# Optimization experiments

Measured on AMD Instinct MI355X. Metric: run time of the kernel, lower is better.

The kernel has to match this reference:

```python
import jax, jax.numpy as jnp
import numpy as np

C = 64
D = C // 8  # query/key channels
B, H, W = 4, 64, 64


def setup_inputs() -> dict:
    key = jax.random.key(0)
    ks = jax.random.split(key, 8)
    x = jax.random.normal(ks[0], (B, C, H, W), dtype=jnp.float32)
    # 1x1 conv params (kernel squeezed to [out_ch, in_ch])
    sq = 1.0 / np.sqrt(C)
    Wq = jax.random.uniform(ks[1], (D, C), jnp.float32, -sq, sq)
    bq = jax.random.uniform(ks[2], (D,), jnp.float32, -sq, sq)
    Wk = jax.random.uniform(ks[3], (D, C), jnp.float32, -sq, sq)
    bk = jax.random.uniform(ks[4], (D,), jnp.float32, -sq, sq)
    Wv = jax.random.uniform(ks[5], (C, C), jnp.float32, -sq, sq)
    bv = jax.random.uniform(ks[6], (C,), jnp.float32, -sq, sq)
    # gamma is zero-initialized in the module; use a nonzero value so the
    # attention path actually contributes to the output.
    gamma = jax.random.normal(ks[7], (1,), dtype=jnp.float32)
    return {"x": x, "Wq": Wq, "bq": bq, "Wk": Wk, "bk": bk, "Wv": Wv, "bv": bv, "gamma": gamma}


def reference(x, Wq, bq, Wk, bk, Wv, bv, gamma):
    b, c, h, w = x.shape
    n = h * w
    xf = x.reshape(b, c, n)                                   # [B,C,N]
    q = jnp.einsum('dc,bcn->bdn', Wq, xf) + bq[None, :, None]  # [B,D,N]
    k = jnp.einsum('dc,bcn->bdn', Wk, xf) + bk[None, :, None]  # [B,D,N]
    v = jnp.einsum('ec,bcn->ben', Wv, xf) + bv[None, :, None]  # [B,C,N]
    energy = jnp.einsum('bdn,bdm->bnm', q, k)                  # [B,N,N] = Q^T K
    attn = jax.nn.softmax(energy, axis=-1)                     # softmax over keys m
    # out[b,c,n] = sum_m v[b,c,m] * attn[b,n,m]  (V @ attention^T in torch)
    out = jnp.einsum('bcm,bnm->bcn', v, attn).reshape(b, c, h, w)
    return gamma[0] * out + x
```

## Files before the change

### kernel.cpp

```cpp
#include <hip/hip_runtime.h>
#include <hip/hip_bf16.h>
#include <math.h>

#define BB 4
#define CC 64
#define DD 8
#define NN 4096
#define KS 8
#define KPS (NN / KS)
#define VSTR 516
#define KSTR 12
#define LOG2E 1.44269504088896340736f

typedef __attribute__((ext_vector_type(4))) short short4v;
typedef __attribute__((ext_vector_type(8))) short short8s;
typedef __attribute__((ext_vector_type(4))) unsigned short ushort4v;
typedef __attribute__((ext_vector_type(8))) unsigned short ushort8;
typedef __attribute__((ext_vector_type(16))) float f32x16;

#if defined(__HIP_DEVICE_COMPILE__)
  #if __has_builtin(__builtin_amdgcn_mfma_f32_32x32x8bf16_1k)
    #define MFMA32x8(A, B, C) __builtin_amdgcn_mfma_f32_32x32x8bf16_1k(A, B, C, 0, 0, 0)
  #elif __has_builtin(__builtin_amdgcn_mfma_f32_32x32x8_bf16)
    #define MFMA32x8(A, B, C) __builtin_amdgcn_mfma_f32_32x32x8_bf16(A, B, C, 0, 0, 0)
  #else
    #error "no 32x32x8 bf16 MFMA builtin in device pass"
  #endif
  #if __has_builtin(__builtin_amdgcn_exp2f)
    #define EXP2(x) __builtin_amdgcn_exp2f(x)
  #else
    #define EXP2(x) exp2f(x)
  #endif
#else
  static __device__ __host__ inline f32x16 MFMA32x8(short4v, short4v, f32x16 c) { return c; }
  #define EXP2(x) exp2f(x)
#endif

static __device__ inline f32x16 PVMFMA(short8s A, short8s B, f32x16 c) {
#if defined(__HIP_DEVICE_COMPILE__) && __has_builtin(__builtin_amdgcn_mfma_f32_32x32x16_bf16)
    typedef __attribute__((ext_vector_type(8))) __bf16 bf16x8;
    return __builtin_amdgcn_mfma_f32_32x32x16_bf16(
        __builtin_bit_cast(bf16x8, A), __builtin_bit_cast(bf16x8, B), c, 0, 0, 0);
#else
    union { short8s v; short4v h[2]; } a, b;
    a.v = A; b.v = B;
    return MFMA32x8(a.h[1], b.h[1], MFMA32x8(a.h[0], b.h[0], c));
#endif
}

static __device__ inline short4v pack4(float a, float b, float c, float d) {
    union { short4v s; __hip_bfloat162 h[2]; } u;
    u.h[0] = __float22bfloat162_rn(make_float2(a, b));
    u.h[1] = __float22bfloat162_rn(make_float2(c, d));
    return u.s;
}
static __device__ inline unsigned packu(float lo, float hi) {
    union { __hip_bfloat162 h; unsigned u; } t;
    t.h = __float22bfloat162_rn(make_float2(lo, hi));
    return t.u;
}

__global__ __launch_bounds__(64) void qkv_kernel(
    const float* __restrict__ x,  const float* __restrict__ Wq, const float* __restrict__ bq,
    const float* __restrict__ Wk, const float* __restrict__ bk,
    const float* __restrict__ Wv, const float* __restrict__ bv,
    unsigned short* __restrict__ qb, unsigned short* __restrict__ kb,
    unsigned short* __restrict__ vT)
{
    __shared__ unsigned short LQ[32 * 8];
    __shared__ unsigned short LK[32 * 8];

    int lane = threadIdx.x & 63;
    int l32 = lane & 31, h2 = lane >> 5;

    int blk = blockIdx.x;
    int b = blk & (BB - 1);
    int ng = blk >> 2;
    int n0 = ng * 32;

    const float* xb = x + (size_t)b * CC * NN + n0 + l32;
    short4v bf[8];
    #pragma unroll
    for (int s = 0; s < 8; ++s) {
        int c0 = s * 8 + 4 * h2;
        float x0 = xb[(size_t)(c0 + 0) * NN];
        float x1 = xb[(size_t)(c0 + 1) * NN];
        float x2 = xb[(size_t)(c0 + 2) * NN];
        float x3 = xb[(size_t)(c0 + 3) * NN];
        bf[s] = pack4(x0, x1, x2, x3);
    }

    #pragma unroll
    for (int rt = 0; rt < 2; ++rt) {
        short4v af[8];
        #pragma unroll
        for (int s = 0; s < 8; ++s) {
            float4 w4 = *(const float4*)(Wv + (size_t)(rt * 32 + l32) * CC + s * 8 + 4 * h2);
            af[s] = pack4(w4.x, w4.y, w4.z, w4.w);
        }
        f32x16 acc;
        #pragma unroll
        for (int r = 0; r < 16; ++r) acc[r] = 0.f;
        #pragma unroll
        for (int s = 0; s < 8; ++s)
            acc = MFMA32x8(af[s], bf[s], acc);
        #pragma unroll
        for (int r = 0; r < 16; ++r) {
            int row = rt * 32 + (r & 3) + 8 * (r >> 2) + 4 * h2;
            float val = acc[r] + bv[row];
            __hip_bfloat16 hv = __float2bfloat16(val);
            vT[((size_t)b * CC + row) * NN + n0 + l32] = *(unsigned short*)&hv;
        }
    }

    {
        short4v af[8];
        #pragma unroll
        for (int s = 0; s < 8; ++s) {
            float4 w4;
            if (l32 < 8) {
                w4 = *(const float4*)(Wq + (size_t)l32 * CC + s * 8 + 4 * h2);
            } else if (l32 < 16) {
                w4 = *(const float4*)(Wk + (size_t)(l32 - 8) * CC + s * 8 + 4 * h2);
            } else {
                w4 = make_float4(0.f, 0.f, 0.f, 0.f);
            }
            af[s] = pack4(w4.x, w4.y, w4.z, w4.w);
        }
        f32x16 acc;
        #pragma unroll
        for (int r = 0; r < 16; ++r) acc[r] = 0.f;
        #pragma unroll
        for (int s = 0; s < 8; ++s)
            acc = MFMA32x8(af[s], bf[s], acc);

        short4v qp = pack4((acc[0] + bq[0 + 4 * h2]) * LOG2E,
                           (acc[1] + bq[1 + 4 * h2]) * LOG2E,
                           (acc[2] + bq[2 + 4 * h2]) * LOG2E,
                           (acc[3] + bq[3 + 4 * h2]) * LOG2E);
        short4v kp = pack4(acc[4] + bk[0 + 4 * h2],
                           acc[5] + bk[1 + 4 * h2],
                           acc[6] + bk[2 + 4 * h2],
                           acc[7] + bk[3 + 4 * h2]);
        *(short4v*)(LQ + (size_t)l32 * 8 + 4 * h2) = qp;
        *(short4v*)(LK + (size_t)l32 * 8 + 4 * h2) = kp;
        __syncthreads();
        int rw = lane & 31;
        if (lane < 32) {
            ushort8 row = *(const ushort8*)(LQ + (size_t)rw * 8);
            *(ushort8*)(qb + ((size_t)b * NN + n0 + rw) * 8) = row;
        } else {
            ushort8 row = *(const ushort8*)(LK + (size_t)rw * 8);
            *(ushort8*)(kb + ((size_t)b * NN + n0 + rw) * 8) = row;
        }
    }
}

__global__ __launch_bounds__(512, 4) void flash_kernel(
    const unsigned short* __restrict__ qb, const unsigned short* __restrict__ kb,
    const unsigned short* __restrict__ vT, unsigned* __restrict__ accb,
    float* __restrict__ sbuf)
{
    __shared__ unsigned short VS[64 * VSTR];
    __shared__ unsigned short KL[512 * KSTR];
    int tid = threadIdx.x;
    int wave = tid >> 6, lane = tid & 63;
    int l32 = lane & 31, h2 = lane >> 5;

    int blk = blockIdx.x;
    int b = blk & (BB - 1);
    int qchunk = (blk >> 2) & 15;
    int split = blk >> 6;
    int n0 = qchunk * 256 + wave * 32;

    short4v qf = *(const short4v*)(qb + ((size_t)b * NN + n0 + l32) * DD + h2 * 4);

    const unsigned short* kbb = kb + (size_t)b * NN * DD;
    const unsigned short* vbb = vT + (size_t)b * CC * NN;
    int m0 = split * KPS;

    {
        int ch = tid >> 3, s8 = (tid & 7) * 8;
        const unsigned short* vg = vbb + (size_t)ch * NN + m0 + s8;
        ushort8 v[8];
        #pragma unroll
        for (int k = 0; k < 8; ++k) v[k] = *(const ushort8*)(vg + 64 * k);
        ushort8 kA = *(const ushort8*)(kbb + (size_t)(m0 + tid) * DD);

        unsigned short* vp = VS + (size_t)ch * VSTR + s8;
        #pragma unroll
        for (int k = 0; k < 8; ++k) {
            *(ushort4v*)(vp + 64 * k)     = *(ushort4v*)&v[k];
            *(ushort4v*)(vp + 64 * k + 4) = *((ushort4v*)&v[k] + 1);
        }
        unsigned short* p = KL + (size_t)tid * KSTR;
        *(ushort4v*)(p)     = *(ushort4v*)&kA;
        *(ushort4v*)(p + 4) = *((ushort4v*)&kA + 1);
    }
    __syncthreads();

    f32x16 o0, o1, zz;
    #pragma unroll
    for (int r = 0; r < 16; ++r) { o0[r] = 0.f; o1[r] = 0.f; zz[r] = 0.f; }
    float s0 = 0.f, s1 = 0.f, s2 = 0.f, s3 = 0.f;

    #pragma unroll
    for (int s = 0; s < 16; ++s) {
        short4v kf = *(const short4v*)(KL + (size_t)(s * 32 + l32) * KSTR + h2 * 4);
        f32x16 st = MFMA32x8(kf, qf, zz);
        float w[16];
        #pragma unroll
        for (int r = 0; r < 16; ++r) w[r] = EXP2(st[r]);
        s0 += (w[0] + w[1]) + (w[2] + w[3]);
        s1 += (w[4] + w[5]) + (w[6] + w[7]);
        s2 += (w[8] + w[9]) + (w[10] + w[11]);
        s3 += (w[12] + w[13]) + (w[14] + w[15]);

        union { short4v s; __hip_bfloat162 h[2]; } u[4];
        #pragma unroll
        for (int g = 0; g < 4; ++g) {
            u[g].h[0] = __float22bfloat162_rn(make_float2(w[4 * g],     w[4 * g + 1]));
            u[g].h[1] = __float22bfloat162_rn(make_float2(w[4 * g + 2], w[4 * g + 3]));
        }
        #pragma unroll
        for (int j = 0; j < 2; ++j) {
            int kb0 = s * 32 + j * 16 + h2 * 4;
            union { short8s v; short4v h[2]; } A, B0, B1;
            A.h[0] = u[2 * j].s;
            A.h[1] = u[2 * j + 1].s;
            B0.h[0] = *(const short4v*)(VS + (size_t)(l32)      * VSTR + kb0);
            B0.h[1] = *(const short4v*)(VS + (size_t)(l32)      * VSTR + kb0 + 8);
            B1.h[0] = *(const short4v*)(VS + (size_t)(32 + l32) * VSTR + kb0);
            B1.h[1] = *(const short4v*)(VS + (size_t)(32 + l32) * VSTR + kb0 + 8);
            o0 = PVMFMA(A.v, B0.v, o0);
            o1 = PVMFMA(A.v, B1.v, o1);
        }
    }

    unsigned* au = accb + (((size_t)((b * KS + split) * 128 + qchunk * 8 + wave)) << 10);
    #pragma unroll
    for (int r = 0; r < 16; ++r)
        au[r * 64 + lane] = packu(o0[r], o1[r]);

    float ssum = (s0 + s1) + (s2 + s3);
    ssum += __shfl_xor(ssum, 32);
    if (lane < 32)
        sbuf[(size_t)(b * KS + split) * NN + n0 + l32] = ssum;
}

__global__ __launch_bounds__(256) void norm_kernel(
    const unsigned* __restrict__ accb, const float* __restrict__ sbuf,
    const float* __restrict__ x, const float* __restrict__ gamma,
    float* __restrict__ out)
{
    __shared__ float tile[16 * 65];
    __shared__ float stl[16];
    int blk = blockIdx.x;
    int t = blk & 7;
    int uu = blk >> 3;
    int b = t & 3;
    int qpar = t >> 2;
    int qhalf = uu & 1;
    int sub = (uu >> 1) & 7;
    int qhi = uu >> 4;
    int qchunk = qhi * 2 + qpar;
    int g32 = qchunk * 8 + sub;
    int n0 = g32 * 32 + qhalf * 16;
    int tid = threadIdx.x;

    if (tid < 16) {
        float st = 0.f;
        #pragma unroll
        for (int sp = 0; sp < KS; ++sp)
            st += sbuf[(size_t)(b * KS + sp) * NN + n0 + tid];
        stl[tid] = 1.0f / st;
    }

    int spoff = tid >> 7;
    int u = tid & 127;
    int rl = u >> 4;
    int lane0 = (u & 15) * 4;

    float alo[4], ahi[4];
    #pragma unroll
    for (int e = 0; e < 4; ++e) { alo[e] = 0.f; ahi[e] = 0.f; }
    #pragma unroll
    for (int p = 0; p < 4; ++p) {
        int sp = p * 2 + spoff;
        const unsigned* base = accb + (((size_t)((b * KS + sp) * 128 + g32)) << 10)
                             + qhalf * 512;
        uint4 v = *(const uint4*)(base + u * 4);
        unsigned wv[4] = {v.x, v.y, v.z, v.w};
        #pragma unroll
        for (int e = 0; e < 4; ++e) {
            alo[e] += __uint_as_float(wv[e] << 16);
            ahi[e] += __uint_as_float(wv[e] & 0xFFFF0000u);
        }
    }

    #pragma unroll
    for (int e = 0; e < 4; ++e) {
        int lane = lane0 + e;
        int h2 = lane >> 5, l32 = lane & 31;
        int ql = (rl & 3) + 8 * ((rl >> 2) & 1) + 4 * h2;
        if (tid < 128) {
            tile[ql * 65 + l32]      = alo[e];
            tile[ql * 65 + 32 + l32] = ahi[e];
        }
    }
    __syncthreads();
    #pragma unroll
    for (int e = 0; e < 4; ++e) {
        int lane = lane0 + e;
        int h2 = lane >> 5, l32 = lane & 31;
        int ql = (rl & 3) + 8 * ((rl >> 2) & 1) + 4 * h2;
        if (tid >= 128) {
            tile[ql * 65 + l32]      += alo[e];
            tile[ql * 65 + 32 + l32] += ahi[e];
        }
    }
    __syncthreads();

    float gm = gamma[0];
    #pragma unroll
    for (int p2 = 0; p2 < 4; ++p2) {
        int idx = p2 * 256 + tid;
        int c = idx >> 4, ql = idx & 15;
        size_t xi = ((size_t)b * CC + c) * NN + n0 + ql;
        out[xi] = gm * tile[ql * 65 + c] * stl[ql] + x[xi];
    }
}

extern "C" void kernel_launch(void* const* d_in, const int* in_sizes, int n_in,
                              void* d_out, int out_size, void* d_ws, size_t ws_size,
                              hipStream_t stream)
{
    const float* x     = (const float*)d_in[0];
    const float* Wq    = (const float*)d_in[1];
    const float* bq    = (const float*)d_in[2];
    const float* Wk    = (const float*)d_in[3];
    const float* bk    = (const float*)d_in[4];
    const float* Wv    = (const float*)d_in[5];
    const float* bv    = (const float*)d_in[6];
    const float* gamma = (const float*)d_in[7];
    float* out = (float*)d_out;

    float* ws = (float*)d_ws;
    size_t off = 0;
    unsigned short* qb = (unsigned short*)(ws + off); off += (size_t)BB * NN * DD / 2 + 64;
    unsigned short* kb = (unsigned short*)(ws + off); off += (size_t)BB * NN * DD / 2 + 64;
    unsigned short* vT = (unsigned short*)(ws + off); off += (size_t)BB * CC * NN / 2 + 64;
    unsigned* accb = (unsigned*)(ws + off); off += (size_t)BB * KS * NN * CC / 2;
    float* sbuf = ws + off; off += (size_t)BB * KS * NN;

    qkv_kernel<<<BB * 128, 64, 0, stream>>>(x, Wq, bq, Wk, bk, Wv, bv, qb, kb, vT);
    flash_kernel<<<KS * 16 * BB, 512, 0, stream>>>(qb, kb, vT, accb, sbuf);
    norm_kernel<<<BB * 256, 256, 0, stream>>>(accb, sbuf, x, gamma, out);
}
```

Baseline: 96.09 us.

## Halve key splits, double-buffer K/V tiles, compute row sums via MFMA

Cuts the number of key splits from 8 to 4, so each flash block now handles two 512-key tiles. The second tile's global loads are issued before computing the first, and it goes into a second shared-memory buffer. Softmax row sums are now produced by an extra MFMA against a ones vector instead of scalar adds. This aims to reduce partial-accumulator traffic in the norm kernel and to hide load latency. In exchange it launches half as many blocks, uses twice the LDS per block (occupancy hint lowered to 2), and adds one MFMA per PV step.

```diff
diff --git a/kernel.cpp b/kernel.cpp
--- a/kernel.cpp
+++ b/kernel.cpp
@@ -6,7 +6,7 @@
 #define CC 64
 #define DD 8
 #define NN 4096
-#define KS 8
+#define KS 4
 #define KPS (NN / KS)
 #define VSTR 516
 #define KSTR 12
@@ -156,13 +156,13 @@
     }
 }
 
-__global__ __launch_bounds__(512, 4) void flash_kernel(
+__global__ __launch_bounds__(512, 2) void flash_kernel(
     const unsigned short* __restrict__ qb, const unsigned short* __restrict__ kb,
     const unsigned short* __restrict__ vT, unsigned* __restrict__ accb,
     float* __restrict__ sbuf)
 {
-    __shared__ unsigned short VS[64 * VSTR];
-    __shared__ unsigned short KL[512 * KSTR];
+    __shared__ unsigned short VS[2][64 * VSTR];
+    __shared__ unsigned short KL[2][512 * KSTR];
     int tid = threadIdx.x;
     int wave = tid >> 6, lane = tid & 63;
     int l32 = lane & 31, h2 = lane >> 5;
@@ -179,73 +179,101 @@
     const unsigned short* vbb = vT + (size_t)b * CC * NN;
     int m0 = split * KPS;
 
+    int ch = tid >> 3, s8 = (tid & 7) * 8;
+    const unsigned short* vg = vbb + (size_t)ch * NN + m0 + s8;
+
     {
-        int ch = tid >> 3, s8 = (tid & 7) * 8;
-        const unsigned short* vg = vbb + (size_t)ch * NN + m0 + s8;
         ushort8 v[8];
         #pragma unroll
         for (int k = 0; k < 8; ++k) v[k] = *(const ushort8*)(vg + 64 * k);
         ushort8 kA = *(const ushort8*)(kbb + (size_t)(m0 + tid) * DD);
 
-        unsigned short* vp = VS + (size_t)ch * VSTR + s8;
+        unsigned short* vp = VS[0] + (size_t)ch * VSTR + s8;
         #pragma unroll
         for (int k = 0; k < 8; ++k) {
             *(ushort4v*)(vp + 64 * k)     = *(ushort4v*)&v[k];
             *(ushort4v*)(vp + 64 * k + 4) = *((ushort4v*)&v[k] + 1);
         }
-        unsigned short* p = KL + (size_t)tid * KSTR;
+        unsigned short* p = KL[0] + (size_t)tid * KSTR;
         *(ushort4v*)(p)     = *(ushort4v*)&kA;
         *(ushort4v*)(p + 4) = *((ushort4v*)&kA + 1);
     }
     __syncthreads();
 
-    f32x16 o0, o1, zz;
-    #pragma unroll
-    for (int r = 0; r < 16; ++r) { o0[r] = 0.f; o1[r] = 0.f; zz[r] = 0.f; }
-    float s0 = 0.f, s1 = 0.f, s2 = 0.f, s3 = 0.f;
-
-    #pragma unroll
-    for (int s = 0; s < 16; ++s) {
-        short4v kf = *(const short4v*)(KL + (size_t)(s * 32 + l32) * KSTR + h2 * 4);
-        f32x16 st = MFMA32x8(kf, qf, zz);
-        float w[16];
-        #pragma unroll
-        for (int r = 0; r < 16; ++r) w[r] = EXP2(st[r]);
-        s0 += (w[0] + w[1]) + (w[2] + w[3]);
-        s1 += (w[4] + w[5]) + (w[6] + w[7]);
-        s2 += (w[8] + w[9]) + (w[10] + w[11]);
-        s3 += (w[12] + w[13]) + (w[14] + w[15]);
-
-        union { short4v s; __hip_bfloat162 h[2]; } u[4];
-        #pragma unroll
-        for (int g = 0; g < 4; ++g) {
-            u[g].h[0] = __float22bfloat162_rn(make_float2(w[4 * g],     w[4 * g + 1]));
-            u[g].h[1] = __float22bfloat162_rn(make_float2(w[4 * g + 2], w[4 * g + 3]));
-        }
-        #pragma unroll
-        for (int j = 0; j < 2; ++j) {
-            int kb0 = s * 32 + j * 16 + h2 * 4;
-            union { short8s v; short4v h[2]; } A, B0, B1;
-            A.h[0] = u[2 * j].s;
-            A.h[1] = u[2 * j + 1].s;
-            B0.h[0] = *(const short4v*)(VS + (size_t)(l32)      * VSTR + kb0);
-            B0.h[1] = *(const short4v*)(VS + (size_t)(l32)      * VSTR + kb0 + 8);
-            B1.h[0] = *(const short4v*)(VS + (size_t)(32 + l32) * VSTR + kb0);
-            B1.h[1] = *(const short4v*)(VS + (size_t)(32 + l32) * VSTR + kb0 + 8);
-            o0 = PVMFMA(A.v, B0.v, o0);
-            o1 = PVMFMA(A.v, B1.v, o1);
-        }
-    }
+    ushort8 v1[8];
+    #pragma unroll
+    for (int k = 0; k < 8; ++k) v1[k] = *(const ushort8*)(vg + 512 + 64 * k);
+    ushort8 kA1 = *(const ushort8*)(kbb + (size_t)(m0 + 512 + tid) * DD);
+
+    union { short8s v; unsigned short e[8]; } ones;
+    #pragma unroll
+    for (int i = 0; i < 8; ++i) ones.e[i] = 0x3F80;
+
+    f32x16 o0, o1, oS, zz;
+    #pragma unroll
+    for (int r = 0; r < 16; ++r) { o0[r] = 0.f; o1[r] = 0.f; oS[r] = 0.f; zz[r] = 0.f; }
+
+#define COMPUTE(ST)                                                              \
+    {                                                                            \
+        _Pragma("unroll")                                                        \
+        for (int s = 0; s < 16; ++s) {                                           \
+            short4v kf = *(const short4v*)(KL[ST] + (size_t)(s * 32 + l32) * KSTR + h2 * 4); \
+            f32x16 sv = MFMA32x8(kf, qf, zz);                                    \
+            float w[16];                                                         \
+            _Pragma("unroll")                                                    \
+            for (int r = 0; r < 16; ++r) w[r] = EXP2(sv[r]);                     \
+            union { short4v s; __hip_bfloat162 h[2]; } u[4];                     \
+            _Pragma("unroll")                                                    \
+            for (int g = 0; g < 4; ++g) {                                        \
+                u[g].h[0] = __float22bfloat162_rn(make_float2(w[4 * g],     w[4 * g + 1])); \
+                u[g].h[1] = __float22bfloat162_rn(make_float2(w[4 * g + 2], w[4 * g + 3])); \
+            }                                                                    \
+            _Pragma("unroll")                                                    \
+            for (int j = 0; j < 2; ++j) {                                        \
+                int kb0 = s * 32 + j * 16 + h2 * 4;                              \
+                union { short8s v; short4v h[2]; } A, B0, B1;                    \
+                A.h[0] = u[2 * j].s;                                             \
+                A.h[1] = u[2 * j + 1].s;                                         \
+                B0.h[0] = *(const short4v*)(VS[ST] + (size_t)(l32)      * VSTR + kb0);     \
+                B0.h[1] = *(const short4v*)(VS[ST] + (size_t)(l32)      * VSTR + kb0 + 8); \
+                B1.h[0] = *(const short4v*)(VS[ST] + (size_t)(32 + l32) * VSTR + kb0);     \
+                B1.h[1] = *(const short4v*)(VS[ST] + (size_t)(32 + l32) * VSTR + kb0 + 8); \
+                o0 = PVMFMA(A.v, B0.v, o0);                                      \
+                o1 = PVMFMA(A.v, B1.v, o1);                                      \
+                oS = PVMFMA(A.v, ones.v, oS);                                    \
+            }                                                                    \
+        }                                                                        \
+    }
+
+    COMPUTE(0)
+
+    {
+        unsigned short* vp = VS[1] + (size_t)ch * VSTR + s8;
+        #pragma unroll
+        for (int k = 0; k < 8; ++k) {
+            *(ushort4v*)(vp + 64 * k)     = *(ushort4v*)&v1[k];
+            *(ushort4v*)(vp + 64 * k + 4) = *((ushort4v*)&v1[k] + 1);
+        }
+        unsigned short* p = KL[1] + (size_t)tid * KSTR;
+        *(ushort4v*)(p)     = *(ushort4v*)&kA1;
+        *(ushort4v*)(p + 4) = *((ushort4v*)&kA1 + 1);
+    }
+    __syncthreads();
+
+    COMPUTE(1)
+#undef COMPUTE
 
     unsigned* au = accb + (((size_t)((b * KS + split) * 128 + qchunk * 8 + wave)) << 10);
     #pragma unroll
     for (int r = 0; r < 16; ++r)
         au[r * 64 + lane] = packu(o0[r], o1[r]);
 
-    float ssum = (s0 + s1) + (s2 + s3);
-    ssum += __shfl_xor(ssum, 32);
-    if (lane < 32)
-        sbuf[(size_t)(b * KS + split) * NN + n0 + l32] = ssum;
+    float* sb = sbuf + (size_t)(b * KS + split) * NN + n0;
+    #pragma unroll
+    for (int r = 0; r < 16; ++r) {
+        int ql = (r & 3) + 8 * (r >> 2) + 4 * h2;
+        if (l32 == r) sb[ql] = oS[r];
+    }
 }
 
 __global__ __launch_bounds__(256) void norm_kernel(
@@ -285,7 +313,7 @@
     #pragma unroll
     for (int e = 0; e < 4; ++e) { alo[e] = 0.f; ahi[e] = 0.f; }
     #pragma unroll
-    for (int p = 0; p < 4; ++p) {
+    for (int p = 0; p < KS / 2; ++p) {
         int sp = p * 2 + spoff;
         const unsigned* base = accb + (((size_t)((b * KS + sp) * 128 + g32)) << 10)
                              + qhalf * 512;
```

Result: faster. 93.79 us (median of 2 runs) (-2.4%).
